# Performance work log

Hardware: AMD Instinct MI355X
Metric: run time of the kernel (lower is better)

The kernel has to match this reference:

```python
import jax, jax.numpy as jnp
import numpy as np

EPS = 1e-5
N_NODES = 10
NUM_JOINTS = 6   # all robot_configs fixed to '3_segments_3DOF' (module's fallback default)
MAX_DOF = 10


def _lin(x, w, b):
    # torch nn.Linear: y = x @ W.T + b, W is (out, in)
    return jnp.einsum('...i,oi->...o', x, w) + b


def _layernorm(x, scale, bias):
    mu = x.mean(-1, keepdims=True)
    var = x.var(-1, keepdims=True)
    return (x - mu) / jnp.sqrt(var + EPS) * scale + bias


def _forward(images, text_lengths, node_features, edge_indices, p):
    B = images.shape[0]
    # --- SimplifiedVLMBackbone ---
    y = jax.lax.conv_general_dilated(images, p['conv_w'], (2, 2), [(3, 3), (3, 3)],
                                     dimension_numbers=('NCHW', 'OIHW', 'NCHW'))
    y = jax.nn.relu(y + p['conv_b'][None, :, None, None])          # (B,32,112,112)
    y = y.reshape(B, 32, 7, 16, 7, 16).mean(axis=(3, 5))            # adaptive avg pool -> (B,32,7,7)
    y = y.reshape(B, 32 * 49)
    y = jax.nn.relu(_lin(y, p['img_fc1_w'], p['img_fc1_b']))
    img_feat = _lin(y, p['img_fc2_w'], p['img_fc2_b'])               # (B,768)
    t = p['text_emb'][jnp.clip(text_lengths, 0, 9999)]               # (B,256)
    vlm = img_feat + _lin(t, p['text_fc_w'], p['text_fc_b'])         # (B,768)

    # --- SoftArmGraphNN ---
    x = jax.nn.relu(_lin(node_features, p['enc1_w'], p['enc1_b']))
    x = _lin(x, p['enc2_w'], p['enc2_b'])                            # (B,N,64)
    src, dst = edge_indices[:, 0, :], edge_indices[:, 1, :]          # (B,E)

    def agg_fn(xi, si, di):
        # mean of neighbor (source) features per destination node; 0 if no neighbors
        g = xi[si]                                                   # (E,D)
        s = jax.ops.segment_sum(g, di, num_segments=N_NODES)
        c = jax.ops.segment_sum(jnp.ones(di.shape, xi.dtype), di, num_segments=N_NODES)
        return s / jnp.maximum(c, 1.0)[:, None]

    for i in range(3):
        residual = x
        mean_nb = jax.vmap(agg_fn)(x, src, dst)                      # (B,N,64)
        comb = jnp.concatenate([x, mean_nb], axis=-1)                # (B,N,128)
        x = _lin(comb, p['gc_w'][i], p['gc_b'][i])
        x = jax.nn.relu(_layernorm(x + residual, p['ln_scale'][i], p['ln_bias'][i]))
    graph_tokens = _lin(x, p['proj_w'], p['proj_b'])                 # (B,N,32)

    # --- AttentionPooling + dual-path fusion ---
    s = _lin(jnp.tanh(_lin(graph_tokens, p['attn1_w'], p['attn1_b'])), p['attn2_w'], p['attn2_b'])
    w = jax.nn.softmax(s, axis=1)                                    # (B,N,1)
    robot_token = jnp.sum(graph_tokens * w, axis=1)                  # (B,32) -> project? 32 vs 768 -> residual add via broadcast pad
    fused = vlm.at[:, :robot_token.shape[-1]].add(robot_token)       # global token residual into vlm features

    # --- NodeActionHead (all samples: 3seg_3DOF -> 6 joints, per-joint MLPs) ---
    comb = jnp.concatenate([
        jnp.broadcast_to(fused[:, None, :], (B, NUM_JOINTS, fused.shape[-1])),
        graph_tokens[:, :NUM_JOINTS, :]], axis=-1)                   # (B,J,800)
    h = jax.nn.relu(jnp.einsum('bjf,jhf->bjh', comb, p['head_w1']) + p['head_b1'])
    h = jax.nn.relu(jnp.einsum('bjf,jhf->bjh', h, p['head_w2']) + p['head_b2'])
    a = jnp.einsum('bjf,jhf->bjh', h, p['head_w3']) + p['head_b3']   # (B,6,16)
    a = jnp.pad(a, ((0, 0), (0, MAX_DOF - NUM_JOINTS), (0, 0)))      # pad to max_dof
    return jnp.transpose(a, (0, 2, 1))                               # (B,16,10)


def setup_inputs() -> dict:
    key = jax.random.key(0)
    ks = iter(jax.random.split(key, 64))

    def nrm(shape, scale=0.02):
        return scale * jax.random.normal(next(ks), shape, dtype=jnp.float32)

    B = 128
    inp = {
        'images': jax.random.normal(next(ks), (B, 3, 224, 224), dtype=jnp.float32),
        'text_lengths': jax.random.randint(next(ks), (B,), 0, 10000, dtype=jnp.int32),
        'node_features': jax.random.normal(next(ks), (B, N_NODES, 19), dtype=jnp.float32),
        'edge_indices': jax.random.randint(next(ks), (B, 2, 18), 0, N_NODES, dtype=jnp.int32),
        'conv_w': nrm((32, 3, 7, 7)), 'conv_b': jnp.zeros(32, jnp.float32),
        'img_fc1_w': nrm((512, 1568)), 'img_fc1_b': jnp.zeros(512, jnp.float32),
        'img_fc2_w': nrm((768, 512)), 'img_fc2_b': jnp.zeros(768, jnp.float32),
        'text_emb': nrm((10000, 256)),
        'text_fc_w': nrm((768, 256)), 'text_fc_b': jnp.zeros(768, jnp.float32),
        'enc1_w': nrm((64, 19)), 'enc1_b': jnp.zeros(64, jnp.float32),
        'enc2_w': nrm((64, 64)), 'enc2_b': jnp.zeros(64, jnp.float32),
        'gc_w': nrm((3, 64, 128)), 'gc_b': jnp.zeros((3, 64), jnp.float32),
        'ln_scale': jnp.ones((3, 64), jnp.float32), 'ln_bias': jnp.zeros((3, 64), jnp.float32),
        'proj_w': nrm((32, 64)), 'proj_b': jnp.zeros(32, jnp.float32),
        'attn1_w': nrm((16, 32)), 'attn1_b': jnp.zeros(16, jnp.float32),
        'attn2_w': nrm((1, 16)), 'attn2_b': jnp.zeros(1, jnp.float32),
        'head_w1': nrm((6, 128, 800)), 'head_b1': jnp.zeros((6, 128), jnp.float32),
        'head_w2': nrm((6, 64, 128)), 'head_b2': jnp.zeros((6, 64), jnp.float32),
        'head_w3': nrm((6, 16, 64)), 'head_b3': jnp.zeros((6, 16), jnp.float32),
    }
    return inp


def reference(images, text_lengths, node_features, edge_indices, conv_w, conv_b,
              img_fc1_w, img_fc1_b, img_fc2_w, img_fc2_b, text_emb, text_fc_w, text_fc_b,
              enc1_w, enc1_b, enc2_w, enc2_b, gc_w, gc_b, ln_scale, ln_bias,
              proj_w, proj_b, attn1_w, attn1_b, attn2_w, attn2_b,
              head_w1, head_b1, head_w2, head_b2, head_w3, head_b3):
    p = dict(conv_w=conv_w, conv_b=conv_b, img_fc1_w=img_fc1_w, img_fc1_b=img_fc1_b,
             img_fc2_w=img_fc2_w, img_fc2_b=img_fc2_b, text_emb=text_emb,
             text_fc_w=text_fc_w, text_fc_b=text_fc_b, enc1_w=enc1_w, enc1_b=enc1_b,
             enc2_w=enc2_w, enc2_b=enc2_b, gc_w=gc_w, gc_b=gc_b, ln_scale=ln_scale,
             ln_bias=ln_bias, proj_w=proj_w, proj_b=proj_b, attn1_w=attn1_w,
             attn1_b=attn1_b, attn2_w=attn2_w, attn2_b=attn2_b, head_w1=head_w1,
             head_b1=head_b1, head_w2=head_w2, head_b2=head_b2, head_w3=head_w3,
             head_b3=head_b3)
    return _forward(images, text_lengths, node_features, edge_indices, p)
```

## Files before the change

### kernel.cpp

```cpp
#include <hip/hip_runtime.h>
#include <hip/hip_bf16.h>
#include <math.h>

typedef __attribute__((ext_vector_type(8))) short bf16x8;
typedef __attribute__((ext_vector_type(4))) float f32x4;

static __device__ __forceinline__ unsigned short f2bf(float f) {
    union { float f; unsigned int u; } x{f};
    unsigned int u = x.u;
    unsigned int r = (u + 0x7fffu + ((u >> 16) & 1u)) >> 16;
    return (unsigned short)r;
}

static __device__ __forceinline__ unsigned int pack2(float f0, float f1) {
    __hip_bfloat162 h = __float22bfloat162_rn(float2{f0, f1});
    union { __hip_bfloat162 h; unsigned int u; } c{h};
    return c.u;
}

__global__ __launch_bounds__(256) void wprep(const float* __restrict__ conv_w,
                                             unsigned short* __restrict__ wB) {
    for (int idx = threadIdx.x; idx < 24 * 32 * 8; idx += 256) {
        int s = idx >> 8;
        int ch = (idx >> 3) & 31;
        int kx = idx & 7;
        int c = s >> 3, ky = s & 7;
        float v = 0.f;
        if (ky < 7 && kx < 7) v = conv_w[ch * 147 + c * 49 + ky * 7 + kx];
        wB[idx] = f2bf(v);
    }
}

#define PSTRIDE 120
__global__ __launch_bounds__(512, 4) void conv_mfma(const float* __restrict__ img,
                                                    const unsigned int* __restrict__ wBu,
                                                    const float* __restrict__ cb,
                                                    float* __restrict__ pooledH) {
    __shared__ unsigned int patch[63 * PSTRIDE];
    const int t = threadIdx.x;
    const int py = blockIdx.x, half = blockIdx.y, b = blockIdx.z;
    const int B = gridDim.z;
    const int lane = t & 63, wid = t >> 6;
    const int r16 = lane & 15, g = lane >> 4;
    const int Y0 = 32 * py + 16 * half - 3;

    const int xc0 = 2 * lane - 3;
    const int xc1 = 2 * lane + 125;
    const int a00 = max(xc0, 0);
    const int a01 = max(xc0 + 1, 0);
    const int a10 = min(xc1, 223);
    const int a11 = min(xc1 + 1, 223);
    const bool v00 = (xc0 >= 0);
    const bool v01 = (xc0 + 1 >= 0);
    const bool v10 = (xc1 <= 223);
    const bool v11 = (xc1 + 1 <= 223);
    const bool c1act = (lane < 52);

    const float* ib = img + (size_t)b * 3 * 224 * 224;

#pragma unroll
    for (int hb = 0; hb < 2; ++hb) {
        float g0[4], g1[4], g2[4], g3[4];
        int rr[4];
        bool rv[4];
#pragma unroll
        for (int i = 0; i < 4; ++i) {
            int r = wid + 8 * (hb * 4 + i);
            int c_ = (r >= 42) ? 2 : ((r >= 21) ? 1 : 0);
            int pr = r - 21 * c_;
            int iy = Y0 + pr;
            rv[i] = (r < 63) & (iy >= 0) & (iy < 224);
            int iyc = min(max(iy, 0), 223);
            const float* rp = ib + (c_ * 224 + iyc) * 224;
            rr[i] = r;
            g0[i] = rp[a00];
            g1[i] = rp[a01];
            g2[i] = rp[a10];
            g3[i] = rp[a11];
        }
#pragma unroll
        for (int i = 0; i < 4; ++i) {
            float f0 = (rv[i] && v00) ? g0[i] : 0.f;
            float f1 = (rv[i] && v01) ? g1[i] : 0.f;
            float f2_ = (rv[i] && v10) ? g2[i] : 0.f;
            float f3 = (rv[i] && v11) ? g3[i] : 0.f;
            if (rr[i] < 63) {
                patch[rr[i] * PSTRIDE + lane] = pack2(f0, f1);
                if (c1act) patch[rr[i] * PSTRIDE + 64 + lane] = pack2(f2_, f3);
            }
        }
    }

    bf16x8 bfrA[6], bfrB[6];
    int rowoff[6];
#pragma unroll
    for (int k = 0; k < 6; ++k) {
        int s = 4 * k + g;
        int c = s >> 3, ky = s & 7;
        int kyc = ky > 6 ? 6 : ky;
        rowoff[k] = c * 21 + kyc;
        union { uint4 q; bf16x8 v; } ua, ub;
        ua.q = *(const uint4*)(wBu + (s * 32 + r16) * 4);
        ub.q = *(const uint4*)(wBu + (s * 32 + r16 + 16) * 4);
        bfrA[k] = ua.v;
        bfrB[k] = ub.v;
    }
    const float biasA = cb[r16], biasB = cb[r16 + 16];

    __syncthreads();

    float accA[7], accB[7];
    int rb[6];
#pragma unroll
    for (int k = 0; k < 6; ++k) rb[k] = (rowoff[k] + 2 * wid) * PSTRIDE;

    for (int t7 = 0; t7 < 7; ++t7) {
        const int oxr = 16 * t7 + r16;
        f32x4 C0 = {biasA, biasA, biasA, biasA};
        f32x4 C1 = {biasB, biasB, biasB, biasB};
#pragma unroll
        for (int k = 0; k < 6; ++k) {
            const unsigned int* ap = &patch[rb[k] + oxr];
            union { unsigned int u[4]; bf16x8 v; } ua;
            ua.u[0] = ap[0];
            ua.u[1] = ap[1];
            ua.u[2] = ap[2];
            ua.u[3] = ap[3];
            C0 = __builtin_amdgcn_mfma_f32_16x16x32_bf16(ua.v, bfrA[k], C0, 0, 0, 0);
            C1 = __builtin_amdgcn_mfma_f32_16x16x32_bf16(ua.v, bfrB[k], C1, 0, 0, 0);
        }
        float s0 = 0.f, s1 = 0.f;
#pragma unroll
        for (int r = 0; r < 4; ++r) {
            s0 += fmaxf(C0[r], 0.f);
            s1 += fmaxf(C1[r], 0.f);
        }
        accA[t7] = s0;
        accB[t7] = s1;
    }
#pragma unroll
    for (int p = 0; p < 7; ++p) {
        accA[p] += __shfl_xor(accA[p], 16);
        accA[p] += __shfl_xor(accA[p], 32);
        accB[p] += __shfl_xor(accB[p], 16);
        accB[p] += __shfl_xor(accB[p], 32);
    }
    __syncthreads();
    float* sw = (float*)patch;
    if (lane < 16) {
#pragma unroll
        for (int p = 0; p < 7; ++p) {
            sw[(wid * 7 + p) * 32 + lane] = accA[p];
            sw[(wid * 7 + p) * 32 + lane + 16] = accB[p];
        }
    }
    __syncthreads();
    if (t < 224) {
        int p = t >> 5, ch = t & 31;
        float s = 0.f;
#pragma unroll
        for (int w = 0; w < 8; ++w) s += sw[(w * 7 + p) * 32 + ch];
        pooledH[(size_t)(half * B + b) * 1568 + ch * 49 + py * 7 + p] = s * (1.f / 256.f);
    }
}

__global__ __launch_bounds__(256) void fc1_k(const float* __restrict__ in,
                                             const float* __restrict__ w,
                                             const float* __restrict__ bias,
                                             float* __restrict__ out, int B) {
    const int t = threadIdx.x, lane = t & 63, wid = t >> 6;
    const int qg = blockIdx.x & 31;
    const int bg = blockIdx.x >> 5;
    const int b0 = bg * 8;
    const int o0 = (qg * 4 + wid) * 4;
    const float4* wp = (const float4*)w;
    const float4* xp0 = (const float4*)in;
    const float4* xp1 = xp0 + (size_t)B * 392;

    float acc[4][8];
#pragma unroll
    for (int oo = 0; oo < 4; ++oo)
#pragma unroll
        for (int r = 0; r < 8; ++r) acc[oo][r] = 0.f;

    for (int i = lane; i < 392; i += 64) {
        float4 wv[4];
#pragma unroll
        for (int oo = 0; oo < 4; ++oo) wv[oo] = wp[(size_t)(o0 + oo) * 392 + i];
#pragma unroll
        for (int r = 0; r < 8; ++r) {
            float4 a = xp0[(size_t)(b0 + r) * 392 + i];
            float4 c = xp1[(size_t)(b0 + r) * 392 + i];
            float4 xv = {a.x + c.x, a.y + c.y, a.z + c.z, a.w + c.w};
#pragma unroll
            for (int oo = 0; oo < 4; ++oo) {
                acc[oo][r] = fmaf(xv.x, wv[oo].x, acc[oo][r]);
                acc[oo][r] = fmaf(xv.y, wv[oo].y, acc[oo][r]);
                acc[oo][r] = fmaf(xv.z, wv[oo].z, acc[oo][r]);
                acc[oo][r] = fmaf(xv.w, wv[oo].w, acc[oo][r]);
            }
        }
    }
#pragma unroll
    for (int oo = 0; oo < 4; ++oo) {
        float v = 0.f;
#pragma unroll
        for (int r = 0; r < 8; ++r) {
            float s = acc[oo][r];
            s += __shfl_xor(s, 32);
            s += __shfl_xor(s, 16);
            s += __shfl_xor(s, 8);
            s += __shfl_xor(s, 4);
            s += __shfl_xor(s, 2);
            s += __shfl_xor(s, 1);
            if (lane == r) v = s;
        }
        if (lane < 8)
            out[(size_t)(b0 + lane) * 512 + o0 + oo] = fmaxf(v + bias[o0 + oo], 0.f);
    }
}

__global__ __launch_bounds__(256) void vlm_k(const float* __restrict__ h1,
                                             const float* __restrict__ w2,
                                             const float* __restrict__ b2,
                                             const int* __restrict__ tlen,
                                             const float* __restrict__ temb,
                                             const float* __restrict__ tw,
                                             const float* __restrict__ tb,
                                             const float* __restrict__ rtok,
                                             float* __restrict__ fused) {
    const int t = threadIdx.x, lane = t & 63, wid = t >> 6;
    const int ogq = blockIdx.x % 48;
    const int bg = blockIdx.x / 48;
    const int b0 = bg * 8;
    const int o0 = (ogq * 4 + wid) * 4;

    int rows[8];
#pragma unroll
    for (int r = 0; r < 8; ++r) {
        int v = tlen[b0 + r];
        rows[r] = min(max(v, 0), 9999);
    }
    const float4* wp = (const float4*)w2;
    const float4* xp = (const float4*)h1;
    const float4* wtp = (const float4*)tw;
    const float4* xtp = (const float4*)temb;

    float acc[4][8];
#pragma unroll
    for (int oo = 0; oo < 4; ++oo)
#pragma unroll
        for (int r = 0; r < 8; ++r) acc[oo][r] = 0.f;

#pragma unroll
    for (int ii = 0; ii < 2; ++ii) {
        int i = lane + (ii << 6);
        float4 wv[4];
#pragma unroll
        for (int oo = 0; oo < 4; ++oo) wv[oo] = wp[(size_t)(o0 + oo) * 128 + i];
#pragma unroll
        for (int r = 0; r < 8; ++r) {
            float4 xv = xp[(size_t)(b0 + r) * 128 + i];
#pragma unroll
            for (int oo = 0; oo < 4; ++oo) {
                acc[oo][r] = fmaf(xv.x, wv[oo].x, acc[oo][r]);
                acc[oo][r] = fmaf(xv.y, wv[oo].y, acc[oo][r]);
                acc[oo][r] = fmaf(xv.z, wv[oo].z, acc[oo][r]);
                acc[oo][r] = fmaf(xv.w, wv[oo].w, acc[oo][r]);
            }
        }
    }
    {
        float4 wv[4];
#pragma unroll
        for (int oo = 0; oo < 4; ++oo) wv[oo] = wtp[(size_t)(o0 + oo) * 64 + lane];
#pragma unroll
        for (int r = 0; r < 8; ++r) {
            float4 xv = xtp[(size_t)rows[r] * 64 + lane];
#pragma unroll
            for (int oo = 0; oo < 4; ++oo) {
                acc[oo][r] = fmaf(xv.x, wv[oo].x, acc[oo][r]);
                acc[oo][r] = fmaf(xv.y, wv[oo].y, acc[oo][r]);
                acc[oo][r] = fmaf(xv.z, wv[oo].z, acc[oo][r]);
                acc[oo][r] = fmaf(xv.w, wv[oo].w, acc[oo][r]);
            }
        }
    }
#pragma unroll
    for (int oo = 0; oo < 4; ++oo) {
        float v = 0.f;
#pragma unroll
        for (int r = 0; r < 8; ++r) {
            float s = acc[oo][r];
            s += __shfl_xor(s, 32);
            s += __shfl_xor(s, 16);
            s += __shfl_xor(s, 8);
            s += __shfl_xor(s, 4);
            s += __shfl_xor(s, 2);
            s += __shfl_xor(s, 1);
            if (lane == r) v = s;
        }
        int o = o0 + oo;
        if (lane < 8) {
            float add = (o < 32) ? rtok[(size_t)(b0 + lane) * 32 + o] : 0.f;
            fused[(size_t)(b0 + lane) * 768 + o] = v + b2[o] + tb[o] + add;
        }
    }
}

__global__ __launch_bounds__(640, 1) void graph_k(
    const float* __restrict__ nfeat, const int* __restrict__ eidx,
    const float* __restrict__ e1w, const float* __restrict__ e1b,
    const float* __restrict__ e2w, const float* __restrict__ e2b,
    const float* __restrict__ gcw, const float* __restrict__ gcb,
    const float* __restrict__ lns, const float* __restrict__ lnb,
    const float* __restrict__ pjw, const float* __restrict__ pjb,
    const float* __restrict__ a1w, const float* __restrict__ a1b,
    const float* __restrict__ a2w, const float* __restrict__ a2b,
    float* __restrict__ gts_g, float* __restrict__ rtok) {
    __shared__ __align__(16) float pool[8448];
    __shared__ __align__(16) float nf[10][20];
    __shared__ __align__(16) float xsA[10][64];
    __shared__ __align__(16) float xsB[10][64];
    __shared__ __align__(16) float nbs[10][64];
    __shared__ __align__(16) float gtss[10][32];
    __shared__ float svs[10];
    __shared__ int se[18], de[18];
    const int t = threadIdx.x;
    const int b = blockIdx.x;
    const int n = t >> 6, o = t & 63;

    if (t < 190) {
        int nn = t / 19, i = t - nn * 19;
        nf[nn][i] = nfeat[(size_t)(b * 10 + nn) * 19 + i];
    }
    if (t < 36) {
        if (t < 18) se[t] = eidx[b * 36 + t];
        else de[t - 18] = eidx[b * 36 + t];
    }
    float* e1wT = pool;
    float* e2wT = pool + 1280;
    for (int u = t; u < 1216; u += 640) {
        int oo = u / 19, k = u - oo * 19;
        e1wT[k * 64 + oo] = e1w[u];
    }
    for (int u = t; u < 4096; u += 640) {
        int oo = u >> 6, k = u & 63;
        e2wT[k * 65 + oo] = e2w[u];
    }
    __syncthreads();

    {
        float acc = e1b[o];
#pragma unroll
        for (int i = 0; i < 19; ++i) acc = fmaf(nf[n][i], e1wT[i * 64 + o], acc);
        xsB[n][o] = fmaxf(acc, 0.f);
    }
    {
        const float* xrow = &xsB[n][0];
        float s0 = 0, s1 = 0, s2 = 0, s3 = 0;
#pragma unroll
        for (int k = 0; k < 64; k += 4) {
            s0 = fmaf(xrow[k], e2wT[k * 65 + o], s0);
            s1 = fmaf(xrow[k + 1], e2wT[(k + 1) * 65 + o], s1);
            s2 = fmaf(xrow[k + 2], e2wT[(k + 2) * 65 + o], s2);
            s3 = fmaf(xrow[k + 3], e2wT[(k + 3) * 65 + o], s3);
        }
        xsA[n][o] = e2b[o] + ((s0 + s1) + (s2 + s3));
    }
    __syncthreads();

    float* src = &xsA[0][0];
    float* dst = &xsB[0][0];
    for (int l = 0; l < 3; ++l) {
        const float* gl = gcw + (size_t)l * 8192;
        for (int u = t; u < 8192; u += 640) {
            int oo = u >> 7, k = u & 127;
            pool[k * 65 + oo] = gl[u];
        }
        {
            float s = 0.f;
            int cnt = 0;
#pragma unroll
            for (int e = 0; e < 18; ++e) {
                bool m = (de[e] == n);
                float v = src[se[e] * 64 + o];
                s += m ? v : 0.f;
                cnt += m ? 1 : 0;
            }
            nbs[n][o] = s / (float)(cnt > 1 ? cnt : 1);
        }
        __syncthreads();
        {
            const float* xa = src + n * 64;
            const float* xb = &nbs[n][0];
            float s0 = 0, s1 = 0, s2 = 0, s3 = 0;
#pragma unroll
            for (int k = 0; k < 64; k += 4) {
                s0 = fmaf(xa[k], pool[k * 65 + o], s0);
                s1 = fmaf(xa[k + 1], pool[(k + 1) * 65 + o], s1);
                s2 = fmaf(xa[k + 2], pool[(k + 2) * 65 + o], s2);
                s3 = fmaf(xa[k + 3], pool[(k + 3) * 65 + o], s3);
            }
#pragma unroll
            for (int k = 0; k < 64; k += 4) {
                s0 = fmaf(xb[k], pool[(64 + k) * 65 + o], s0);
                s1 = fmaf(xb[k + 1], pool[(64 + k + 1) * 65 + o], s1);
                s2 = fmaf(xb[k + 2], pool[(64 + k + 2) * 65 + o], s2);
                s3 = fmaf(xb[k + 3], pool[(64 + k + 3) * 65 + o], s3);
            }
            float v = gcb[l * 64 + o] + ((s0 + s1) + (s2 + s3)) + xa[o];
            float mu = v;
            mu += __shfl_xor(mu, 32);
            mu += __shfl_xor(mu, 16);
            mu += __shfl_xor(mu, 8);
            mu += __shfl_xor(mu, 4);
            mu += __shfl_xor(mu, 2);
            mu += __shfl_xor(mu, 1);
            mu *= (1.f / 64.f);
            float d = v - mu;
            float vr = d * d;
            vr += __shfl_xor(vr, 32);
            vr += __shfl_xor(vr, 16);
            vr += __shfl_xor(vr, 8);
            vr += __shfl_xor(vr, 4);
            vr += __shfl_xor(vr, 2);
            vr += __shfl_xor(vr, 1);
            vr *= (1.f / 64.f);
            dst[n * 64 + o] =
                fmaxf(d / sqrtf(vr + 1e-5f) * lns[l * 64 + o] + lnb[l * 64 + o], 0.f);
        }
        __syncthreads();
        float* tmp = src;
        src = dst;
        dst = tmp;
    }

    float* pjwT = pool;
    float* a1wT = pool + 2112;
    for (int u = t; u < 2048; u += 640) {
        int oo = u >> 6, k = u & 63;
        pjwT[k * 33 + oo] = pjw[u];
    }
    for (int u = t; u < 512; u += 640) {
        int hh = u >> 5, k = u & 31;
        a1wT[k * 17 + hh] = a1w[u];
    }
    __syncthreads();

    if (o < 32) {
        const float* xrow = src + n * 64;
        float s0 = 0, s1 = 0, s2 = 0, s3 = 0;
#pragma unroll
        for (int k = 0; k < 64; k += 4) {
            s0 = fmaf(xrow[k], pjwT[k * 33 + o], s0);
            s1 = fmaf(xrow[k + 1], pjwT[(k + 1) * 33 + o], s1);
            s2 = fmaf(xrow[k + 2], pjwT[(k + 2) * 33 + o], s2);
            s3 = fmaf(xrow[k + 3], pjwT[(k + 3) * 33 + o], s3);
        }
        float gv = pjb[o] + ((s0 + s1) + (s2 + s3));
        gtss[n][o] = gv;
        gts_g[(size_t)b * 320 + n * 32 + o] = gv;
    }
    if (o < 16) {
        const float* xrow = &gtss[n][0];
        float s0 = 0, s1 = 0, s2 = 0, s3 = 0;
#pragma unroll
        for (int k = 0; k < 32; k += 4) {
            s0 = fmaf(xrow[k], a1wT[k * 17 + o], s0);
            s1 = fmaf(xrow[k + 1], a1wT[(k + 1) * 17 + o], s1);
            s2 = fmaf(xrow[k + 2], a1wT[(k + 2) * 17 + o], s2);
            s3 = fmaf(xrow[k + 3], a1wT[(k + 3) * 17 + o], s3);
        }
        float z = a1b[o] + ((s0 + s1) + (s2 + s3));
        float sc = tanhf(z) * a2w[o];
        sc += __shfl_xor(sc, 8);
        sc += __shfl_xor(sc, 4);
        sc += __shfl_xor(sc, 2);
        sc += __shfl_xor(sc, 1);
        if (o == 0) svs[n] = sc + a2b[0];
    }
    __syncthreads();

    if (n == 0 && o < 32) {
        float m = svs[0];
#pragma unroll
        for (int i = 1; i < 10; ++i) m = fmaxf(m, svs[i]);
        float e[10];
        float sum = 0.f;
#pragma unroll
        for (int i = 0; i < 10; ++i) {
            e[i] = expf(svs[i] - m);
            sum += e[i];
        }
        float inv = 1.f / sum;
        float rt = 0.f;
#pragma unroll
        for (int nn = 0; nn < 10; ++nn) rt = fmaf(gtss[nn][o], e[nn] * inv, rt);
        rtok[(size_t)b * 32 + o] = rt;
    }
}

__global__ __launch_bounds__(256) void head1_k(const float* __restrict__ fused,
                                               const float* __restrict__ gts,
                                               const float* __restrict__ w1,
                                               const float* __restrict__ b1,
                                               float* __restrict__ h1T) {
    const int t = threadIdx.x, lane = t & 63, wid = t >> 6;
    const int ogq = blockIdx.x % 48;
    const int bg = blockIdx.x / 48;
    const int b0 = bg * 8;
    const int j = ogq >> 3;
    const int o0 = ogq * 16 + wid * 4;
    const float4* wp = (const float4*)w1;
    const float4* fp = (const float4*)fused;
    const float4* gp = (const float4*)gts;

    float acc[4][8];
#pragma unroll
    for (int oo = 0; oo < 4; ++oo)
#pragma unroll
        for (int r = 0; r < 8; ++r) acc[oo][r] = 0.f;

    for (int i = lane; i < 200; i += 64) {
        float4 wv[4];
#pragma unroll
        for (int oo = 0; oo < 4; ++oo) wv[oo] = wp[(size_t)(o0 + oo) * 200 + i];
#pragma unroll
        for (int r = 0; r < 8; ++r) {
            float4 xv = (i < 192) ? fp[(size_t)(b0 + r) * 192 + i]
                                  : gp[(size_t)(b0 + r) * 80 + j * 8 + (i - 192)];
#pragma unroll
            for (int oo = 0; oo < 4; ++oo) {
                acc[oo][r] = fmaf(xv.x, wv[oo].x, acc[oo][r]);
                acc[oo][r] = fmaf(xv.y, wv[oo].y, acc[oo][r]);
                acc[oo][r] = fmaf(xv.z, wv[oo].z, acc[oo][r]);
                acc[oo][r] = fmaf(xv.w, wv[oo].w, acc[oo][r]);
            }
        }
    }
#pragma unroll
    for (int oo = 0; oo < 4; ++oo) {
        float v = 0.f;
#pragma unroll
        for (int r = 0; r < 8; ++r) {
            float s = acc[oo][r];
            s += __shfl_xor(s, 32);
            s += __shfl_xor(s, 16);
            s += __shfl_xor(s, 8);
            s += __shfl_xor(s, 4);
            s += __shfl_xor(s, 2);
            s += __shfl_xor(s, 1);
            if (lane == r) v = s;
        }
        int o = o0 + oo;
        if (lane < 8) h1T[(size_t)o * 128 + b0 + lane] = fmaxf(v + b1[o], 0.f);
    }
}

__global__ __launch_bounds__(128) void head2_k(const float* __restrict__ h1T,
                                               const float* __restrict__ w2,
                                               const float* __restrict__ b2,
                                               float* __restrict__ h2T) {
    const int o2 = blockIdx.x;
    const int j = o2 >> 6;
    const int b = threadIdx.x;
    const float* wrow = w2 + (size_t)o2 * 128;
    const float* xcol = h1T + (size_t)j * 128 * 128 + b;
    float acc = b2[o2];
#pragma unroll 16
    for (int k = 0; k < 128; ++k) acc = fmaf(xcol[k * 128], wrow[k], acc);
    h2T[(size_t)o2 * 128 + b] = fmaxf(acc, 0.f);
}

__global__ __launch_bounds__(128) void head3_k(const float* __restrict__ h2T,
                                               const float* __restrict__ w3,
                                               const float* __restrict__ b3,
                                               float* __restrict__ out) {
    const int jj = blockIdx.x % 10;
    const int oo = blockIdx.x / 10;
    const int b = threadIdx.x;
    float acc = 0.f;
    if (jj < 6) {
        const float* wrow = w3 + (size_t)(jj * 16 + oo) * 64;
        const float* xcol = h2T + (size_t)jj * 64 * 128 + b;
        acc = b3[jj * 16 + oo];
#pragma unroll 16
        for (int k = 0; k < 64; ++k) acc = fmaf(xcol[k * 128], wrow[k], acc);
    }
    out[(size_t)b * 160 + oo * 10 + jj] = acc;
}

extern "C" void kernel_launch(void* const* d_in, const int* in_sizes, int n_in,
                              void* d_out, int out_size, void* d_ws, size_t ws_size,
                              hipStream_t stream) {
    const float* images = (const float*)d_in[0];
    const int* tlen = (const int*)d_in[1];
    const float* nfeat = (const float*)d_in[2];
    const int* eidx = (const int*)d_in[3];
    const float* conv_w = (const float*)d_in[4];
    const float* conv_b = (const float*)d_in[5];
    const float* fc1w = (const float*)d_in[6];
    const float* fc1b = (const float*)d_in[7];
    const float* fc2w = (const float*)d_in[8];
    const float* fc2b = (const float*)d_in[9];
    const float* temb = (const float*)d_in[10];
    const float* tfw = (const float*)d_in[11];
    const float* tfb = (const float*)d_in[12];
    const float* e1w = (const float*)d_in[13];
    const float* e1b = (const float*)d_in[14];
    const float* e2w = (const float*)d_in[15];
    const float* e2b = (const float*)d_in[16];
    const float* gcw = (const float*)d_in[17];
    const float* gcb = (const float*)d_in[18];
    const float* lns = (const float*)d_in[19];
    const float* lnb = (const float*)d_in[20];
    const float* pjw = (const float*)d_in[21];
    const float* pjb = (const float*)d_in[22];
    const float* a1w = (const float*)d_in[23];
    const float* a1b = (const float*)d_in[24];
    const float* a2w = (const float*)d_in[25];
    const float* a2b = (const float*)d_in[26];
    const float* w1 = (const float*)d_in[27];
    const float* b1 = (const float*)d_in[28];
    const float* w2 = (const float*)d_in[29];
    const float* b2 = (const float*)d_in[30];
    const float* w3 = (const float*)d_in[31];
    const float* b3 = (const float*)d_in[32];

    const int B = in_sizes[0] / (3 * 224 * 224);

    float* ws = (float*)d_ws;
    unsigned short* wB = (unsigned short*)d_ws;
    float* pooledH = ws + 3072;
    float* h1fc = pooledH + (size_t)2 * B * 1568;
    float* fused = h1fc + (size_t)B * 512;
    float* gts = fused + (size_t)B * 768;
    float* rtok = gts + (size_t)B * 320;
    float* h1T = pooledH;
    float* h2T = pooledH + 98304;

    wprep<<<1, 256, 0, stream>>>(conv_w, wB);
    conv_mfma<<<dim3(7, 2, B), 512, 0, stream>>>(images, (const unsigned int*)wB,
                                                 conv_b, pooledH);
    fc1_k<<<512, 256, 0, stream>>>(pooledH, fc1w, fc1b, h1fc, B);
    graph_k<<<B, 640, 0, stream>>>(nfeat, eidx, e1w, e1b, e2w, e2b, gcw, gcb,
                                   lns, lnb, pjw, pjb, a1w, a1b, a2w, a2b,
                                   gts, rtok);
    vlm_k<<<768, 256, 0, stream>>>(h1fc, fc2w, fc2b, tlen, temb, tfw, tfb,
                                   rtok, fused);
    head1_k<<<768, 256, 0, stream>>>(fused, gts, w1, b1, h1T);
    head2_k<<<384, 128, 0, stream>>>(h1T, w2, b2, h2T);
    head3_k<<<160, 128, 0, stream>>>(h2T, w3, b3, (float*)d_out);
}
```

Before: 128.0 us.

## Fuse weight prep into graph kernel, merge head2/head3, duplicate conv patch for aligned LDS

The conv weight bf16 conversion moves into an extra block of the graph kernel, which now runs first, so one launch is removed. head2 and head3 are merged into a single kernel that keeps the intermediate activations in shared memory and zeroes the padded output columns. The conv kernel stores a second copy of the patch shifted by one element, so every lane can read its A fragment with 8-byte aligned loads. The cost is double the patch shared memory, which may lower occupancy, and only 48 blocks for the fused heads kernel.

```diff
diff --git a/kernel.cpp b/kernel.cpp
--- a/kernel.cpp
+++ b/kernel.cpp
@@ -18,297 +18,8 @@
     return c.u;
 }
 
-__global__ __launch_bounds__(256) void wprep(const float* __restrict__ conv_w,
-                                             unsigned short* __restrict__ wB) {
-    for (int idx = threadIdx.x; idx < 24 * 32 * 8; idx += 256) {
-        int s = idx >> 8;
-        int ch = (idx >> 3) & 31;
-        int kx = idx & 7;
-        int c = s >> 3, ky = s & 7;
-        float v = 0.f;
-        if (ky < 7 && kx < 7) v = conv_w[ch * 147 + c * 49 + ky * 7 + kx];
-        wB[idx] = f2bf(v);
-    }
-}
-
-#define PSTRIDE 120
-__global__ __launch_bounds__(512, 4) void conv_mfma(const float* __restrict__ img,
-                                                    const unsigned int* __restrict__ wBu,
-                                                    const float* __restrict__ cb,
-                                                    float* __restrict__ pooledH) {
-    __shared__ unsigned int patch[63 * PSTRIDE];
-    const int t = threadIdx.x;
-    const int py = blockIdx.x, half = blockIdx.y, b = blockIdx.z;
-    const int B = gridDim.z;
-    const int lane = t & 63, wid = t >> 6;
-    const int r16 = lane & 15, g = lane >> 4;
-    const int Y0 = 32 * py + 16 * half - 3;
-
-    const int xc0 = 2 * lane - 3;
-    const int xc1 = 2 * lane + 125;
-    const int a00 = max(xc0, 0);
-    const int a01 = max(xc0 + 1, 0);
-    const int a10 = min(xc1, 223);
-    const int a11 = min(xc1 + 1, 223);
-    const bool v00 = (xc0 >= 0);
-    const bool v01 = (xc0 + 1 >= 0);
-    const bool v10 = (xc1 <= 223);
-    const bool v11 = (xc1 + 1 <= 223);
-    const bool c1act = (lane < 52);
-
-    const float* ib = img + (size_t)b * 3 * 224 * 224;
-
-#pragma unroll
-    for (int hb = 0; hb < 2; ++hb) {
-        float g0[4], g1[4], g2[4], g3[4];
-        int rr[4];
-        bool rv[4];
-#pragma unroll
-        for (int i = 0; i < 4; ++i) {
-            int r = wid + 8 * (hb * 4 + i);
-            int c_ = (r >= 42) ? 2 : ((r >= 21) ? 1 : 0);
-            int pr = r - 21 * c_;
-            int iy = Y0 + pr;
-            rv[i] = (r < 63) & (iy >= 0) & (iy < 224);
-            int iyc = min(max(iy, 0), 223);
-            const float* rp = ib + (c_ * 224 + iyc) * 224;
-            rr[i] = r;
-            g0[i] = rp[a00];
-            g1[i] = rp[a01];
-            g2[i] = rp[a10];
-            g3[i] = rp[a11];
-        }
-#pragma unroll
-        for (int i = 0; i < 4; ++i) {
-            float f0 = (rv[i] && v00) ? g0[i] : 0.f;
-            float f1 = (rv[i] && v01) ? g1[i] : 0.f;
-            float f2_ = (rv[i] && v10) ? g2[i] : 0.f;
-            float f3 = (rv[i] && v11) ? g3[i] : 0.f;
-            if (rr[i] < 63) {
-                patch[rr[i] * PSTRIDE + lane] = pack2(f0, f1);
-                if (c1act) patch[rr[i] * PSTRIDE + 64 + lane] = pack2(f2_, f3);
-            }
-        }
-    }
-
-    bf16x8 bfrA[6], bfrB[6];
-    int rowoff[6];
-#pragma unroll
-    for (int k = 0; k < 6; ++k) {
-        int s = 4 * k + g;
-        int c = s >> 3, ky = s & 7;
-        int kyc = ky > 6 ? 6 : ky;
-        rowoff[k] = c * 21 + kyc;
-        union { uint4 q; bf16x8 v; } ua, ub;
-        ua.q = *(const uint4*)(wBu + (s * 32 + r16) * 4);
-        ub.q = *(const uint4*)(wBu + (s * 32 + r16 + 16) * 4);
-        bfrA[k] = ua.v;
-        bfrB[k] = ub.v;
-    }
-    const float biasA = cb[r16], biasB = cb[r16 + 16];
-
-    __syncthreads();
-
-    float accA[7], accB[7];
-    int rb[6];
-#pragma unroll
-    for (int k = 0; k < 6; ++k) rb[k] = (rowoff[k] + 2 * wid) * PSTRIDE;
-
-    for (int t7 = 0; t7 < 7; ++t7) {
-        const int oxr = 16 * t7 + r16;
-        f32x4 C0 = {biasA, biasA, biasA, biasA};
-        f32x4 C1 = {biasB, biasB, biasB, biasB};
-#pragma unroll
-        for (int k = 0; k < 6; ++k) {
-            const unsigned int* ap = &patch[rb[k] + oxr];
-            union { unsigned int u[4]; bf16x8 v; } ua;
-            ua.u[0] = ap[0];
-            ua.u[1] = ap[1];
-            ua.u[2] = ap[2];
-            ua.u[3] = ap[3];
-            C0 = __builtin_amdgcn_mfma_f32_16x16x32_bf16(ua.v, bfrA[k], C0, 0, 0, 0);
-            C1 = __builtin_amdgcn_mfma_f32_16x16x32_bf16(ua.v, bfrB[k], C1, 0, 0, 0);
-        }
-        float s0 = 0.f, s1 = 0.f;
-#pragma unroll
-        for (int r = 0; r < 4; ++r) {
-            s0 += fmaxf(C0[r], 0.f);
-            s1 += fmaxf(C1[r], 0.f);
-        }
-        accA[t7] = s0;
-        accB[t7] = s1;
-    }
-#pragma unroll
-    for (int p = 0; p < 7; ++p) {
-        accA[p] += __shfl_xor(accA[p], 16);
-        accA[p] += __shfl_xor(accA[p], 32);
-        accB[p] += __shfl_xor(accB[p], 16);
-        accB[p] += __shfl_xor(accB[p], 32);
-    }
-    __syncthreads();
-    float* sw = (float*)patch;
-    if (lane < 16) {
-#pragma unroll
-        for (int p = 0; p < 7; ++p) {
-            sw[(wid * 7 + p) * 32 + lane] = accA[p];
-            sw[(wid * 7 + p) * 32 + lane + 16] = accB[p];
-        }
-    }
-    __syncthreads();
-    if (t < 224) {
-        int p = t >> 5, ch = t & 31;
-        float s = 0.f;
-#pragma unroll
-        for (int w = 0; w < 8; ++w) s += sw[(w * 7 + p) * 32 + ch];
-        pooledH[(size_t)(half * B + b) * 1568 + ch * 49 + py * 7 + p] = s * (1.f / 256.f);
-    }
-}
-
-__global__ __launch_bounds__(256) void fc1_k(const float* __restrict__ in,
-                                             const float* __restrict__ w,
-                                             const float* __restrict__ bias,
-                                             float* __restrict__ out, int B) {
-    const int t = threadIdx.x, lane = t & 63, wid = t >> 6;
-    const int qg = blockIdx.x & 31;
-    const int bg = blockIdx.x >> 5;
-    const int b0 = bg * 8;
-    const int o0 = (qg * 4 + wid) * 4;
-    const float4* wp = (const float4*)w;
-    const float4* xp0 = (const float4*)in;
-    const float4* xp1 = xp0 + (size_t)B * 392;
-
-    float acc[4][8];
-#pragma unroll
-    for (int oo = 0; oo < 4; ++oo)
-#pragma unroll
-        for (int r = 0; r < 8; ++r) acc[oo][r] = 0.f;
-
-    for (int i = lane; i < 392; i += 64) {
-        float4 wv[4];
-#pragma unroll
-        for (int oo = 0; oo < 4; ++oo) wv[oo] = wp[(size_t)(o0 + oo) * 392 + i];
-#pragma unroll
-        for (int r = 0; r < 8; ++r) {
-            float4 a = xp0[(size_t)(b0 + r) * 392 + i];
-            float4 c = xp1[(size_t)(b0 + r) * 392 + i];
-            float4 xv = {a.x + c.x, a.y + c.y, a.z + c.z, a.w + c.w};
-#pragma unroll
-            for (int oo = 0; oo < 4; ++oo) {
-                acc[oo][r] = fmaf(xv.x, wv[oo].x, acc[oo][r]);
-                acc[oo][r] = fmaf(xv.y, wv[oo].y, acc[oo][r]);
-                acc[oo][r] = fmaf(xv.z, wv[oo].z, acc[oo][r]);
-                acc[oo][r] = fmaf(xv.w, wv[oo].w, acc[oo][r]);
-            }
-        }
-    }
-#pragma unroll
-    for (int oo = 0; oo < 4; ++oo) {
-        float v = 0.f;
-#pragma unroll
-        for (int r = 0; r < 8; ++r) {
-            float s = acc[oo][r];
-            s += __shfl_xor(s, 32);
-            s += __shfl_xor(s, 16);
-            s += __shfl_xor(s, 8);
-            s += __shfl_xor(s, 4);
-            s += __shfl_xor(s, 2);
-            s += __shfl_xor(s, 1);
-            if (lane == r) v = s;
-        }
-        if (lane < 8)
-            out[(size_t)(b0 + lane) * 512 + o0 + oo] = fmaxf(v + bias[o0 + oo], 0.f);
-    }
-}
-
-__global__ __launch_bounds__(256) void vlm_k(const float* __restrict__ h1,
-                                             const float* __restrict__ w2,
-                                             const float* __restrict__ b2,
-                                             const int* __restrict__ tlen,
-                                             const float* __restrict__ temb,
-                                             const float* __restrict__ tw,
-                                             const float* __restrict__ tb,
-                                             const float* __restrict__ rtok,
-                                             float* __restrict__ fused) {
-    const int t = threadIdx.x, lane = t & 63, wid = t >> 6;
-    const int ogq = blockIdx.x % 48;
-    const int bg = blockIdx.x / 48;
-    const int b0 = bg * 8;
-    const int o0 = (ogq * 4 + wid) * 4;
-
-    int rows[8];
-#pragma unroll
-    for (int r = 0; r < 8; ++r) {
-        int v = tlen[b0 + r];
-        rows[r] = min(max(v, 0), 9999);
-    }
-    const float4* wp = (const float4*)w2;
-    const float4* xp = (const float4*)h1;
-    const float4* wtp = (const float4*)tw;
-    const float4* xtp = (const float4*)temb;
-
-    float acc[4][8];
-#pragma unroll
-    for (int oo = 0; oo < 4; ++oo)
-#pragma unroll
-        for (int r = 0; r < 8; ++r) acc[oo][r] = 0.f;
-
-#pragma unroll
-    for (int ii = 0; ii < 2; ++ii) {
-        int i = lane + (ii << 6);
-        float4 wv[4];
-#pragma unroll
-        for (int oo = 0; oo < 4; ++oo) wv[oo] = wp[(size_t)(o0 + oo) * 128 + i];
-#pragma unroll
-        for (int r = 0; r < 8; ++r) {
-            float4 xv = xp[(size_t)(b0 + r) * 128 + i];
-#pragma unroll
-            for (int oo = 0; oo < 4; ++oo) {
-                acc[oo][r] = fmaf(xv.x, wv[oo].x, acc[oo][r]);
-                acc[oo][r] = fmaf(xv.y, wv[oo].y, acc[oo][r]);
-                acc[oo][r] = fmaf(xv.z, wv[oo].z, acc[oo][r]);
-                acc[oo][r] = fmaf(xv.w, wv[oo].w, acc[oo][r]);
-            }
-        }
-    }
-    {
-        float4 wv[4];
-#pragma unroll
-        for (int oo = 0; oo < 4; ++oo) wv[oo] = wtp[(size_t)(o0 + oo) * 64 + lane];
-#pragma unroll
-        for (int r = 0; r < 8; ++r) {
-            float4 xv = xtp[(size_t)rows[r] * 64 + lane];
-#pragma unroll
-            for (int oo = 0; oo < 4; ++oo) {
-                acc[oo][r] = fmaf(xv.x, wv[oo].x, acc[oo][r]);
-                acc[oo][r] = fmaf(xv.y, wv[oo].y, acc[oo][r]);
-                acc[oo][r] = fmaf(xv.z, wv[oo].z, acc[oo][r]);
-                acc[oo][r] = fmaf(xv.w, wv[oo].w, acc[oo][r]);
-            }
-        }
-    }
-#pragma unroll
-    for (int oo = 0; oo < 4; ++oo) {
-        float v = 0.f;
-#pragma unroll
-        for (int r = 0; r < 8; ++r) {
-            float s = acc[oo][r];
-            s += __shfl_xor(s, 32);
-            s += __shfl_xor(s, 16);
-            s += __shfl_xor(s, 8);
-            s += __shfl_xor(s, 4);
-            s += __shfl_xor(s, 2);
-            s += __shfl_xor(s, 1);
-            if (lane == r) v = s;
-        }
-        int o = o0 + oo;
-        if (lane < 8) {
-            float add = (o < 32) ? rtok[(size_t)(b0 + lane) * 32 + o] : 0.f;
-            fused[(size_t)(b0 + lane) * 768 + o] = v + b2[o] + tb[o] + add;
-        }
-    }
-}
-
-__global__ __launch_bounds__(640, 1) void graph_k(
+__global__ __launch_bounds__(640, 1) void graph_wprep(
+    const float* __restrict__ conv_w, unsigned short* __restrict__ wB,
     const float* __restrict__ nfeat, const int* __restrict__ eidx,
     const float* __restrict__ e1w, const float* __restrict__ e1b,
     const float* __restrict__ e2w, const float* __restrict__ e2b,
@@ -317,7 +28,7 @@
     const float* __restrict__ pjw, const float* __restrict__ pjb,
     const float* __restrict__ a1w, const float* __restrict__ a1b,
     const float* __restrict__ a2w, const float* __restrict__ a2b,
-    float* __restrict__ gts_g, float* __restrict__ rtok) {
+    float* __restrict__ gts_g, float* __restrict__ rtok, int B) {
     __shared__ __align__(16) float pool[8448];
     __shared__ __align__(16) float nf[10][20];
     __shared__ __align__(16) float xsA[10][64];
@@ -329,6 +40,19 @@
     const int t = threadIdx.x;
     const int b = blockIdx.x;
     const int n = t >> 6, o = t & 63;
+
+    if (b == B) {
+        for (int idx = t; idx < 24 * 32 * 8; idx += 640) {
+            int s = idx >> 8;
+            int ch = (idx >> 3) & 31;
+            int kx = idx & 7;
+            int c = s >> 3, ky = s & 7;
+            float v = 0.f;
+            if (ky < 7 && kx < 7) v = conv_w[ch * 147 + c * 49 + ky * 7 + kx];
+            wB[idx] = f2bf(v);
+        }
+        return;
+    }
 
     if (t < 190) {
         int nn = t / 19, i = t - nn * 19;
@@ -501,6 +225,294 @@
     }
 }
 
+#define PSTRIDE 120
+#define PHALF (63 * PSTRIDE)
+__global__ __launch_bounds__(512, 4) void conv_mfma(const float* __restrict__ img,
+                                                    const unsigned int* __restrict__ wBu,
+                                                    const float* __restrict__ cb,
+                                                    float* __restrict__ pooledH) {
+    __shared__ __align__(16) unsigned int patch[2 * PHALF];
+    const int t = threadIdx.x;
+    const int py = blockIdx.x, half = blockIdx.y, b = blockIdx.z;
+    const int B = gridDim.z;
+    const int lane = t & 63, wid = t >> 6;
+    const int r16 = lane & 15, g = lane >> 4;
+    const int Y0 = 32 * py + 16 * half - 3;
+
+    const int xc0 = 2 * lane - 3;
+    const int xc1 = 2 * lane + 125;
+    const int a00 = max(xc0, 0);
+    const int a01 = max(xc0 + 1, 0);
+    const int a10 = min(xc1, 223);
+    const int a11 = min(xc1 + 1, 223);
+    const bool v00 = (xc0 >= 0);
+    const bool v01 = (xc0 + 1 >= 0);
+    const bool v10 = (xc1 <= 223);
+    const bool v11 = (xc1 + 1 <= 223);
+    const bool c1act = (lane < 52);
+
+    const float* ib = img + (size_t)b * 3 * 224 * 224;
+
+#pragma unroll
+    for (int hb = 0; hb < 2; ++hb) {
+        float g0[4], g1[4], g2[4], g3[4];
+        int rr[4];
+        bool rv[4];
+#pragma unroll
+        for (int i = 0; i < 4; ++i) {
+            int r = wid + 8 * (hb * 4 + i);
+            int c_ = (r >= 42) ? 2 : ((r >= 21) ? 1 : 0);
+            int pr = r - 21 * c_;
+            int iy = Y0 + pr;
+            rv[i] = (r < 63) & (iy >= 0) & (iy < 224);
+            int iyc = min(max(iy, 0), 223);
+            const float* rp = ib + (c_ * 224 + iyc) * 224;
+            rr[i] = r;
+            g0[i] = rp[a00];
+            g1[i] = rp[a01];
+            g2[i] = rp[a10];
+            g3[i] = rp[a11];
+        }
+#pragma unroll
+        for (int i = 0; i < 4; ++i) {
+            float f0 = (rv[i] && v00) ? g0[i] : 0.f;
+            float f1 = (rv[i] && v01) ? g1[i] : 0.f;
+            float f2_ = (rv[i] && v10) ? g2[i] : 0.f;
+            float f3 = (rv[i] && v11) ? g3[i] : 0.f;
+            if (rr[i] < 63) {
+                unsigned int v01p = pack2(f0, f1);
+                unsigned int v23p = pack2(f2_, f3);
+                patch[rr[i] * PSTRIDE + lane] = v01p;
+                if (lane >= 1) patch[PHALF + rr[i] * PSTRIDE + lane - 1] = v01p;
+                if (c1act) {
+                    patch[rr[i] * PSTRIDE + 64 + lane] = v23p;
+                    patch[PHALF + rr[i] * PSTRIDE + 63 + lane] = v23p;
+                }
+            }
+        }
+    }
+
+    bf16x8 bfrA[6], bfrB[6];
+    int rowoff[6];
+#pragma unroll
+    for (int k = 0; k < 6; ++k) {
+        int s = 4 * k + g;
+        int c = s >> 3, ky = s & 7;
+        int kyc = ky > 6 ? 6 : ky;
+        rowoff[k] = c * 21 + kyc;
+        union { uint4 q; bf16x8 v; } ua, ub;
+        ua.q = *(const uint4*)(wBu + (s * 32 + r16) * 4);
+        ub.q = *(const uint4*)(wBu + (s * 32 + r16 + 16) * 4);
+        bfrA[k] = ua.v;
+        bfrB[k] = ub.v;
+    }
+    const float biasA = cb[r16], biasB = cb[r16 + 16];
+
+    __syncthreads();
+
+    const int sel = r16 & 1;
+    const unsigned int* pbase = patch + sel * PHALF;
+    float accA[7], accB[7];
+    int rb[6];
+#pragma unroll
+    for (int k = 0; k < 6; ++k) rb[k] = (rowoff[k] + 2 * wid) * PSTRIDE;
+
+    for (int t7 = 0; t7 < 7; ++t7) {
+        const int idx0 = 16 * t7 + r16 - sel;
+        f32x4 C0 = {biasA, biasA, biasA, biasA};
+        f32x4 C1 = {biasB, biasB, biasB, biasB};
+#pragma unroll
+        for (int k = 0; k < 6; ++k) {
+            const uint2* ap2 = (const uint2*)(pbase + rb[k] + idx0);
+            uint2 q0 = ap2[0];
+            uint2 q1 = ap2[1];
+            union { unsigned int u[4]; bf16x8 v; } ua;
+            ua.u[0] = q0.x;
+            ua.u[1] = q0.y;
+            ua.u[2] = q1.x;
+            ua.u[3] = q1.y;
+            C0 = __builtin_amdgcn_mfma_f32_16x16x32_bf16(ua.v, bfrA[k], C0, 0, 0, 0);
+            C1 = __builtin_amdgcn_mfma_f32_16x16x32_bf16(ua.v, bfrB[k], C1, 0, 0, 0);
+        }
+        float s0 = 0.f, s1 = 0.f;
+#pragma unroll
+        for (int r = 0; r < 4; ++r) {
+            s0 += fmaxf(C0[r], 0.f);
+            s1 += fmaxf(C1[r], 0.f);
+        }
+        accA[t7] = s0;
+        accB[t7] = s1;
+    }
+#pragma unroll
+    for (int p = 0; p < 7; ++p) {
+        accA[p] += __shfl_xor(accA[p], 16);
+        accA[p] += __shfl_xor(accA[p], 32);
+        accB[p] += __shfl_xor(accB[p], 16);
+        accB[p] += __shfl_xor(accB[p], 32);
+    }
+    __syncthreads();
+    float* sw = (float*)patch;
+    if (lane < 16) {
+#pragma unroll
+        for (int p = 0; p < 7; ++p) {
+            sw[(wid * 7 + p) * 32 + lane] = accA[p];
+            sw[(wid * 7 + p) * 32 + lane + 16] = accB[p];
+        }
+    }
+    __syncthreads();
+    if (t < 224) {
+        int p = t >> 5, ch = t & 31;
+        float s = 0.f;
+#pragma unroll
+        for (int w = 0; w < 8; ++w) s += sw[(w * 7 + p) * 32 + ch];
+        pooledH[(size_t)(half * B + b) * 1568 + ch * 49 + py * 7 + p] = s * (1.f / 256.f);
+    }
+}
+
+__global__ __launch_bounds__(256) void fc1_k(const float* __restrict__ in,
+                                             const float* __restrict__ w,
+                                             const float* __restrict__ bias,
+                                             float* __restrict__ out, int B) {
+    const int t = threadIdx.x, lane = t & 63, wid = t >> 6;
+    const int qg = blockIdx.x & 31;
+    const int bg = blockIdx.x >> 5;
+    const int b0 = bg * 8;
+    const int o0 = (qg * 4 + wid) * 4;
+    const float4* wp = (const float4*)w;
+    const float4* xp0 = (const float4*)in;
+    const float4* xp1 = xp0 + (size_t)B * 392;
+
+    float acc[4][8];
+#pragma unroll
+    for (int oo = 0; oo < 4; ++oo)
+#pragma unroll
+        for (int r = 0; r < 8; ++r) acc[oo][r] = 0.f;
+
+    for (int i = lane; i < 392; i += 64) {
+        float4 wv[4];
+#pragma unroll
+        for (int oo = 0; oo < 4; ++oo) wv[oo] = wp[(size_t)(o0 + oo) * 392 + i];
+#pragma unroll
+        for (int r = 0; r < 8; ++r) {
+            float4 a = xp0[(size_t)(b0 + r) * 392 + i];
+            float4 c = xp1[(size_t)(b0 + r) * 392 + i];
+            float4 xv = {a.x + c.x, a.y + c.y, a.z + c.z, a.w + c.w};
+#pragma unroll
+            for (int oo = 0; oo < 4; ++oo) {
+                acc[oo][r] = fmaf(xv.x, wv[oo].x, acc[oo][r]);
+                acc[oo][r] = fmaf(xv.y, wv[oo].y, acc[oo][r]);
+                acc[oo][r] = fmaf(xv.z, wv[oo].z, acc[oo][r]);
+                acc[oo][r] = fmaf(xv.w, wv[oo].w, acc[oo][r]);
+            }
+        }
+    }
+#pragma unroll
+    for (int oo = 0; oo < 4; ++oo) {
+        float v = 0.f;
+#pragma unroll
+        for (int r = 0; r < 8; ++r) {
+            float s = acc[oo][r];
+            s += __shfl_xor(s, 32);
+            s += __shfl_xor(s, 16);
+            s += __shfl_xor(s, 8);
+            s += __shfl_xor(s, 4);
+            s += __shfl_xor(s, 2);
+            s += __shfl_xor(s, 1);
+            if (lane == r) v = s;
+        }
+        if (lane < 8)
+            out[(size_t)(b0 + lane) * 512 + o0 + oo] = fmaxf(v + bias[o0 + oo], 0.f);
+    }
+}
+
+__global__ __launch_bounds__(256) void vlm_k(const float* __restrict__ h1,
+                                             const float* __restrict__ w2,
+                                             const float* __restrict__ b2,
+                                             const int* __restrict__ tlen,
+                                             const float* __restrict__ temb,
+                                             const float* __restrict__ tw,
+                                             const float* __restrict__ tb,
+                                             const float* __restrict__ rtok,
+                                             float* __restrict__ fused) {
+    const int t = threadIdx.x, lane = t & 63, wid = t >> 6;
+    const int ogq = blockIdx.x % 48;
+    const int bg = blockIdx.x / 48;
+    const int b0 = bg * 8;
+    const int o0 = (ogq * 4 + wid) * 4;
+
+    int rows[8];
+#pragma unroll
+    for (int r = 0; r < 8; ++r) {
+        int v = tlen[b0 + r];
+        rows[r] = min(max(v, 0), 9999);
+    }
+    const float4* wp = (const float4*)w2;
+    const float4* xp = (const float4*)h1;
+    const float4* wtp = (const float4*)tw;
+    const float4* xtp = (const float4*)temb;
+
+    float acc[4][8];
+#pragma unroll
+    for (int oo = 0; oo < 4; ++oo)
+#pragma unroll
+        for (int r = 0; r < 8; ++r) acc[oo][r] = 0.f;
+
+#pragma unroll
+    for (int ii = 0; ii < 2; ++ii) {
+        int i = lane + (ii << 6);
+        float4 wv[4];
+#pragma unroll
+        for (int oo = 0; oo < 4; ++oo) wv[oo] = wp[(size_t)(o0 + oo) * 128 + i];
+#pragma unroll
+        for (int r = 0; r < 8; ++r) {
+            float4 xv = xp[(size_t)(b0 + r) * 128 + i];
+#pragma unroll
+            for (int oo = 0; oo < 4; ++oo) {
+                acc[oo][r] = fmaf(xv.x, wv[oo].x, acc[oo][r]);
+                acc[oo][r] = fmaf(xv.y, wv[oo].y, acc[oo][r]);
+                acc[oo][r] = fmaf(xv.z, wv[oo].z, acc[oo][r]);
+                acc[oo][r] = fmaf(xv.w, wv[oo].w, acc[oo][r]);
+            }
+        }
+    }
+    {
+        float4 wv[4];
+#pragma unroll
+        for (int oo = 0; oo < 4; ++oo) wv[oo] = wtp[(size_t)(o0 + oo) * 64 + lane];
+#pragma unroll
+        for (int r = 0; r < 8; ++r) {
+            float4 xv = xtp[(size_t)rows[r] * 64 + lane];
+#pragma unroll
+            for (int oo = 0; oo < 4; ++oo) {
+                acc[oo][r] = fmaf(xv.x, wv[oo].x, acc[oo][r]);
+                acc[oo][r] = fmaf(xv.y, wv[oo].y, acc[oo][r]);
+                acc[oo][r] = fmaf(xv.z, wv[oo].z, acc[oo][r]);
+                acc[oo][r] = fmaf(xv.w, wv[oo].w, acc[oo][r]);
+            }
+        }
+    }
+#pragma unroll
+    for (int oo = 0; oo < 4; ++oo) {
+        float v = 0.f;
+#pragma unroll
+        for (int r = 0; r < 8; ++r) {
+            float s = acc[oo][r];
+            s += __shfl_xor(s, 32);
+            s += __shfl_xor(s, 16);
+            s += __shfl_xor(s, 8);
+            s += __shfl_xor(s, 4);
+            s += __shfl_xor(s, 2);
+            s += __shfl_xor(s, 1);
+            if (lane == r) v = s;
+        }
+        int o = o0 + oo;
+        if (lane < 8) {
+            float add = (o < 32) ? rtok[(size_t)(b0 + lane) * 32 + o] : 0.f;
+            fused[(size_t)(b0 + lane) * 768 + o] = v + b2[o] + tb[o] + add;
+        }
+    }
+}
+
 __global__ __launch_bounds__(256) void head1_k(const float* __restrict__ fused,
                                                const float* __restrict__ gts,
                                                const float* __restrict__ w1,
@@ -558,37 +570,59 @@
     }
 }
 
-__global__ __launch_bounds__(128) void head2_k(const float* __restrict__ h1T,
-                                               const float* __restrict__ w2,
-                                               const float* __restrict__ b2,
-                                               float* __restrict__ h2T) {
-    const int o2 = blockIdx.x;
-    const int j = o2 >> 6;
-    const int b = threadIdx.x;
-    const float* wrow = w2 + (size_t)o2 * 128;
-    const float* xcol = h1T + (size_t)j * 128 * 128 + b;
-    float acc = b2[o2];
-#pragma unroll 16
-    for (int k = 0; k < 128; ++k) acc = fmaf(xcol[k * 128], wrow[k], acc);
-    h2T[(size_t)o2 * 128 + b] = fmaxf(acc, 0.f);
-}
-
-__global__ __launch_bounds__(128) void head3_k(const float* __restrict__ h2T,
-                                               const float* __restrict__ w3,
-                                               const float* __restrict__ b3,
-                                               float* __restrict__ out) {
-    const int jj = blockIdx.x % 10;
-    const int oo = blockIdx.x / 10;
-    const int b = threadIdx.x;
-    float acc = 0.f;
-    if (jj < 6) {
-        const float* wrow = w3 + (size_t)(jj * 16 + oo) * 64;
-        const float* xcol = h2T + (size_t)jj * 64 * 128 + b;
-        acc = b3[jj * 16 + oo];
-#pragma unroll 16
-        for (int k = 0; k < 64; ++k) acc = fmaf(xcol[k * 128], wrow[k], acc);
-    }
-    out[(size_t)b * 160 + oo * 10 + jj] = acc;
+__global__ __launch_bounds__(128) void heads23_k(const float* __restrict__ h1T,
+                                                 const float* __restrict__ w2,
+                                                 const float* __restrict__ b2,
+                                                 const float* __restrict__ w3,
+                                                 const float* __restrict__ b3,
+                                                 float* __restrict__ out) {
+    __shared__ float h2s[64][17];
+    const int j = blockIdx.x >> 3;
+    const int bg = blockIdx.x & 7;
+    const int t = threadIdx.x;
+    const int bl = t & 15, og = t >> 4;
+    const int b = bg * 16 + bl;
+
+#pragma unroll
+    for (int oi = 0; oi < 8; ++oi) {
+        const int o2 = og * 8 + oi;
+        const float* wrow = w2 + (size_t)(j * 64 + o2) * 128;
+        const float* xcol = h1T + (size_t)j * 16384 + b;
+        float s0 = 0, s1 = 0, s2 = 0, s3 = 0;
+#pragma unroll
+        for (int k = 0; k < 128; k += 4) {
+            s0 = fmaf(xcol[k * 128], wrow[k], s0);
+            s1 = fmaf(xcol[(k + 1) * 128], wrow[k + 1], s1);
+            s2 = fmaf(xcol[(k + 2) * 128], wrow[k + 2], s2);
+            s3 = fmaf(xcol[(k + 3) * 128], wrow[k + 3], s3);
+        }
+        h2s[o2][bl] = fmaxf(b2[j * 64 + o2] + ((s0 + s1) + (s2 + s3)), 0.f);
+    }
+    __syncthreads();
+#pragma unroll
+    for (int oi = 0; oi < 2; ++oi) {
+        const int oo = og * 2 + oi;
+        const float* wrow = w3 + (size_t)(j * 16 + oo) * 64;
+        float s0 = 0, s1 = 0, s2 = 0, s3 = 0;
+#pragma unroll
+        for (int k = 0; k < 64; k += 4) {
+            s0 = fmaf(h2s[k][bl], wrow[k], s0);
+            s1 = fmaf(h2s[k + 1][bl], wrow[k + 1], s1);
+            s2 = fmaf(h2s[k + 2][bl], wrow[k + 2], s2);
+            s3 = fmaf(h2s[k + 3][bl], wrow[k + 3], s3);
+        }
+        out[(size_t)b * 160 + oo * 10 + j] =
+            b3[j * 16 + oo] + ((s0 + s1) + (s2 + s3));
+    }
+    if (j == 0) {
+        for (int u = t; u < 16 * 16 * 4; u += 128) {
+            int bb = u & 15;
+            int rest = u >> 4;
+            int oo = rest & 15;
+            int jj = 6 + (rest >> 4);
+            out[(size_t)(bg * 16 + bb) * 160 + oo * 10 + jj] = 0.f;
+        }
+    }
 }
 
 extern "C" void kernel_launch(void* const* d_in, const int* in_sizes, int n_in,
@@ -638,18 +672,16 @@
     float* gts = fused + (size_t)B * 768;
     float* rtok = gts + (size_t)B * 320;
     float* h1T = pooledH;
-    float* h2T = pooledH + 98304;
-
-    wprep<<<1, 256, 0, stream>>>(conv_w, wB);
+
+    graph_wprep<<<B + 1, 640, 0, stream>>>(conv_w, wB, nfeat, eidx,
+                                           e1w, e1b, e2w, e2b, gcw, gcb,
+                                           lns, lnb, pjw, pjb, a1w, a1b,
+                                           a2w, a2b, gts, rtok, B);
     conv_mfma<<<dim3(7, 2, B), 512, 0, stream>>>(images, (const unsigned int*)wB,
                                                  conv_b, pooledH);
     fc1_k<<<512, 256, 0, stream>>>(pooledH, fc1w, fc1b, h1fc, B);
-    graph_k<<<B, 640, 0, stream>>>(nfeat, eidx, e1w, e1b, e2w, e2b, gcw, gcb,
-                                   lns, lnb, pjw, pjb, a1w, a1b, a2w, a2b,
-                                   gts, rtok);
     vlm_k<<<768, 256, 0, stream>>>(h1fc, fc2w, fc2b, tlen, temb, tfw, tfb,
                                    rtok, fused);
     head1_k<<<768, 256, 0, stream>>>(fused, gts, w1, b1, h1T);
-    head2_k<<<384, 128, 0, stream>>>(h1T, w2, b2, h2T);
-    head3_k<<<160, 128, 0, stream>>>(h2T, w3, b3, (float*)d_out);
-}
+    heads23_k<<<48, 128, 0, stream>>>(h1T, w2, b2, w3, b3, (float*)d_out);
+}
```

Result: slower. 149.3 us (+16.6%).
